# Kernel tuning notes

Measured on AMD Instinct MI355X. Metric: run time of the kernel, lower is better.

The kernel has to match this reference:

```python
import jax, jax.numpy as jnp
import numpy as np

# Standard H36M 32-joint kinematic tree (parent of each joint; -1 = root/hip).
# parents[j] < j for all j, so joints can be processed in index order.
PARENTS = [-1, 0, 1, 2, 3, 4, 0, 6, 7, 8, 9, 0, 11, 12, 13, 14,
           12, 16, 17, 18, 19, 20, 19, 22, 12, 24, 25, 26, 27, 28, 27, 30]
NUM_JOINTS = 32
BATCH = 262144


def setup_inputs() -> dict:
    key = jax.random.key(0)
    k1, k2 = jax.random.split(key)
    angles = jax.random.normal(k1, (BATCH, NUM_JOINTS, 3, 3), dtype=jnp.float32)
    offsets = jax.random.normal(k2, (NUM_JOINTS, 3), dtype=jnp.float32)
    return {"angles": angles, "offsets": offsets}


def reference(angles, offsets):
    """Batched forward kinematics over the H36M 32-joint tree.

    angles:  [B, 32, 3, 3] local joint rotation matrices
    offsets: [32, 3]       bone offset (row) vectors
    returns: [B, 32, 3]    global joint positions (getJointPositions analogue)
    """
    B = angles.shape[0]
    pos = [None] * NUM_JOINTS
    rot = [None] * NUM_JOINTS
    # Root (hip): position zero, global rotation = local hip rotation.
    pos[0] = jnp.zeros((B, 3), dtype=angles.dtype)
    rot[0] = angles[:, 0]
    # Fixed-size loop over the kinematic chain (31 joints); batch dim vectorized.
    for j in range(1, NUM_JOINTS):
        p = PARENTS[j]
        # offset[j] (row vector) @ parent global rotation + parent position
        pos[j] = jnp.einsum('k,bkl->bl', offsets[j], rot[p]) + pos[p]
        # local rotation @ parent global rotation
        rot[j] = jnp.einsum('bik,bkl->bil', angles[:, j], rot[p])
    return jnp.stack(pos, axis=1)  # [B, 32, 3]
```

## Files before the change

### kernel.cpp

```cpp
#include <hip/hip_runtime.h>


#define ASM_VMCNT9() asm volatile("s_waitcnt vmcnt(9)" ::: "memory")
#define ASM_VMCNT0() asm volatile("s_waitcnt vmcnt(0)" ::: "memory")
#define ASM_LGKM0()  asm volatile("s_waitcnt lgkmcnt(0)" ::: "memory")

__global__ __launch_bounds__(256) void fk32_kernel(
    const float* __restrict__ angles,
    const float* __restrict__ offsets,
    float* __restrict__ out,
    int B)
{
    constexpr int PAR[32] = {-1,0,1,2,3,4,0,6,7,8,9,0,11,12,13,14,
                             12,16,17,18,19,20,19,22,12,24,25,26,27,28,27,30};

    const int wid   = threadIdx.x >> 6;
    const int lane  = threadIdx.x & 63;
    const int wbase = blockIdx.x * 256 + wid * 64;
    const int b     = wbase + lane;

    __shared__ float4 lds[2][4][576];

    const float4* __restrict__ gbase =
        reinterpret_cast<const float4*>(angles) + (size_t)wbase * 72u;

    const float4* gp[9];
#pragma unroll
    for (int t = 0; t < 9; ++t) {
        const int n = t * 64 + lane;
        const int e = n / 9;
        const int q = n - e * 9;
        gp[t] = gbase + (e * 72 + q);
    }

#pragma unroll
    for (int t = 0; t < 9; ++t)
        __builtin_amdgcn_global_load_lds(
            (const __attribute__((address_space(1))) void*)(gp[t]),
            (__attribute__((address_space(3))) void*)(&lds[0][wid][t * 64]),
            16, 0, 0);

    float rot[32][3][3];
    float pos[32][3];

#pragma unroll
    for (int g = 0; g < 8; ++g) {
        if (g < 7) {
            ASM_LGKM0();
#pragma unroll
            for (int t = 0; t < 9; ++t)
                __builtin_amdgcn_global_load_lds(
                    (const __attribute__((address_space(1))) void*)(gp[t] + 9 * (g + 1)),
                    (__attribute__((address_space(3))) void*)(&lds[(g + 1) & 1][wid][t * 64]),
                    16, 0, 0);
        }
        if (g == 7) { ASM_VMCNT0(); } else { ASM_VMCNT9(); }

        float a[36];
#pragma unroll
        for (int q = 0; q < 9; ++q) {
            const float4 v = lds[g & 1][wid][lane * 9 + q];
            a[4*q+0] = v.x; a[4*q+1] = v.y; a[4*q+2] = v.z; a[4*q+3] = v.w;
        }

#pragma unroll
        for (int jj = 0; jj < 4; ++jj) {
            const int j = g * 4 + jj;
            if (j == 0) {
#pragma unroll
                for (int i = 0; i < 3; ++i)
#pragma unroll
                    for (int l = 0; l < 3; ++l)
                        rot[0][i][l] = a[i*3 + l];
                pos[0][0] = 0.f; pos[0][1] = 0.f; pos[0][2] = 0.f;
            } else {
                const int p = PAR[j];
                const float o0 = offsets[j*3+0];
                const float o1 = offsets[j*3+1];
                const float o2 = offsets[j*3+2];
#pragma unroll
                for (int l = 0; l < 3; ++l)
                    pos[j][l] = fmaf(o0, rot[p][0][l],
                               fmaf(o1, rot[p][1][l],
                               fmaf(o2, rot[p][2][l], pos[p][l])));
#pragma unroll
                for (int i = 0; i < 3; ++i) {
                    const float a0 = a[jj*9 + i*3 + 0];
                    const float a1 = a[jj*9 + i*3 + 1];
                    const float a2 = a[jj*9 + i*3 + 2];
#pragma unroll
                    for (int l = 0; l < 3; ++l)
                        rot[j][i][l] = fmaf(a0, rot[p][0][l],
                                      fmaf(a1, rot[p][1][l],
                                           a2 * rot[p][2][l]));
                }
            }
        }
    }

    float4* __restrict__ op = reinterpret_cast<float4*>(out) + (size_t)b * 24u;
#pragma unroll
    for (int g = 0; g < 8; ++g) {
        op[g*3+0] = make_float4(pos[g*4+0][0], pos[g*4+0][1], pos[g*4+0][2], pos[g*4+1][0]);
        op[g*3+1] = make_float4(pos[g*4+1][1], pos[g*4+1][2], pos[g*4+2][0], pos[g*4+2][1]);
        op[g*3+2] = make_float4(pos[g*4+2][2], pos[g*4+3][0], pos[g*4+3][1], pos[g*4+3][2]);
    }
}

extern "C" void kernel_launch(void* const* d_in, const int* in_sizes, int n_in,
                              void* d_out, int out_size, void* d_ws, size_t ws_size,
                              hipStream_t stream) {
    const float* angles  = (const float*)d_in[0];
    const float* offsets = (const float*)d_in[1];
    float* out = (float*)d_out;
    const int B = in_sizes[0] / 288;
    const int block = 256;
    const int grid = (B + block - 1) / block;
    fk32_kernel<<<grid, block, 0, stream>>>(angles, offsets, out, B);
}
```

Measured before the change: 444.9 us.

## Stage output through LDS for coalesced stores and use single-wave blocks

Each lane's joint positions are written into a padded LDS buffer, and the two halves of the output are flushed with coalesced float4 stores at the midpoint and at the end. Before, every lane wrote 24 strided float4s directly to global memory. Blocks shrink to one wavefront of 64 threads, which removes the multi-wave LDS partitioning. The vmcnt wait at g==4 is adjusted to account for the 12 stores issued at g==3. The grid no longer rounds up, which assumes B is a multiple of 64, and the mid-loop stores may interfere with the vmcnt accounting.

After: 433.8 us. 2.5% less time.

```diff
diff --git a/kernel.cpp b/kernel.cpp
--- a/kernel.cpp
+++ b/kernel.cpp
@@ -1,11 +1,10 @@
 #include <hip/hip_runtime.h>
 
 
-#define ASM_VMCNT9() asm volatile("s_waitcnt vmcnt(9)" ::: "memory")
-#define ASM_VMCNT0() asm volatile("s_waitcnt vmcnt(0)" ::: "memory")
+#define ASM_VMCNT(N) asm volatile("s_waitcnt vmcnt(" #N ")" ::: "memory")
 #define ASM_LGKM0()  asm volatile("s_waitcnt lgkmcnt(0)" ::: "memory")
 
-__global__ __launch_bounds__(256) void fk32_kernel(
+__global__ __launch_bounds__(64) void fk32_kernel(
     const float* __restrict__ angles,
     const float* __restrict__ offsets,
     float* __restrict__ out,
@@ -14,15 +13,16 @@
     constexpr int PAR[32] = {-1,0,1,2,3,4,0,6,7,8,9,0,11,12,13,14,
                              12,16,17,18,19,20,19,22,12,24,25,26,27,28,27,30};
 
-    const int wid   = threadIdx.x >> 6;
-    const int lane  = threadIdx.x & 63;
-    const int wbase = blockIdx.x * 256 + wid * 64;
-    const int b     = wbase + lane;
+    const int lane  = threadIdx.x;
+    const int wbase = blockIdx.x * 64;
 
-    __shared__ float4 lds[2][4][576];
+    __shared__ float4 lin[2][576];
+    __shared__ float4 lout[832];
 
     const float4* __restrict__ gbase =
         reinterpret_cast<const float4*>(angles) + (size_t)wbase * 72u;
+    float4* __restrict__ gout =
+        reinterpret_cast<float4*>(out) + (size_t)wbase * 24u;
 
     const float4* gp[9];
 #pragma unroll
@@ -37,7 +37,7 @@
     for (int t = 0; t < 9; ++t)
         __builtin_amdgcn_global_load_lds(
             (const __attribute__((address_space(1))) void*)(gp[t]),
-            (__attribute__((address_space(3))) void*)(&lds[0][wid][t * 64]),
+            (__attribute__((address_space(3))) void*)(&lin[0][t * 64]),
             16, 0, 0);
 
     float rot[32][3][3];
@@ -51,15 +51,17 @@
             for (int t = 0; t < 9; ++t)
                 __builtin_amdgcn_global_load_lds(
                     (const __attribute__((address_space(1))) void*)(gp[t] + 9 * (g + 1)),
-                    (__attribute__((address_space(3))) void*)(&lds[(g + 1) & 1][wid][t * 64]),
+                    (__attribute__((address_space(3))) void*)(&lin[(g + 1) & 1][t * 64]),
                     16, 0, 0);
         }
-        if (g == 7) { ASM_VMCNT0(); } else { ASM_VMCNT9(); }
+        if (g == 7)      { ASM_VMCNT(0);  }
+        else if (g == 4) { ASM_VMCNT(21); }
+        else             { ASM_VMCNT(9);  }
 
         float a[36];
 #pragma unroll
         for (int q = 0; q < 9; ++q) {
-            const float4 v = lds[g & 1][wid][lane * 9 + q];
+            const float4 v = lin[g & 1][lane * 9 + q];
             a[4*q+0] = v.x; a[4*q+1] = v.y; a[4*q+2] = v.z; a[4*q+3] = v.w;
         }
 
@@ -96,14 +98,26 @@
                 }
             }
         }
-    }
 
-    float4* __restrict__ op = reinterpret_cast<float4*>(out) + (size_t)b * 24u;
+        {
+            const int gg = g & 3;
+            const int j0 = g * 4;
+            lout[lane*13 + gg*3 + 0] = make_float4(pos[j0+0][0], pos[j0+0][1], pos[j0+0][2], pos[j0+1][0]);
+            lout[lane*13 + gg*3 + 1] = make_float4(pos[j0+1][1], pos[j0+1][2], pos[j0+2][0], pos[j0+2][1]);
+            lout[lane*13 + gg*3 + 2] = make_float4(pos[j0+2][2], pos[j0+3][0], pos[j0+3][1], pos[j0+3][2]);
+        }
+
+        if (g == 3 || g == 7) {
+            const int h = (g == 3) ? 0 : 1;
 #pragma unroll
-    for (int g = 0; g < 8; ++g) {
-        op[g*3+0] = make_float4(pos[g*4+0][0], pos[g*4+0][1], pos[g*4+0][2], pos[g*4+1][0]);
-        op[g*3+1] = make_float4(pos[g*4+1][1], pos[g*4+1][2], pos[g*4+2][0], pos[g*4+2][1]);
-        op[g*3+2] = make_float4(pos[g*4+2][2], pos[g*4+3][0], pos[g*4+3][1], pos[g*4+3][2]);
+            for (int s = 0; s < 12; ++s) {
+                const int n = s * 64 + lane;
+                const int e = n / 12;
+                const int q = n - e * 12;
+                const float4 v = lout[e*13 + q];
+                gout[e*24 + h*12 + q] = v;
+            }
+        }
     }
 }
 
@@ -114,7 +128,7 @@
     const float* offsets = (const float*)d_in[1];
     float* out = (float*)d_out;
     const int B = in_sizes[0] / 288;
-    const int block = 256;
-    const int grid = (B + block - 1) / block;
+    const int block = 64;
+    const int grid = B / block;
     fk32_kernel<<<grid, block, 0, stream>>>(angles, offsets, out, B);
 }
```
